# Kernel optimization log

Hardware: AMD Instinct MI355X
Metric: run time of the kernel (lower is better)

## Reference

```python
import jax, jax.numpy as jnp
import numpy as np

N, C, T, V = 16, 192, 120, 100
HEADS = 4
HEAD_CH = C // HEADS  # 48


def setup_inputs() -> dict:
    key = jax.random.key(0)
    ks = jax.random.split(key, 10)
    s = 0.05
    return {
        "x_q": jax.random.normal(ks[0], (N, C, T, V), jnp.float32),
        "x_kv": jax.random.normal(ks[1], (N, C, T, V), jnp.float32),
        "wq": jax.random.normal(ks[2], (C, C), jnp.float32) * s,
        "bq": jax.random.normal(ks[3], (C,), jnp.float32) * s,
        "wk": jax.random.normal(ks[4], (C, C), jnp.float32) * s,
        "bk": jax.random.normal(ks[5], (C,), jnp.float32) * s,
        "wp": jax.random.normal(ks[6], (C, C * HEADS), jnp.float32) * s,
        "bp": jax.random.normal(ks[7], (C,), jnp.float32) * s,
        "alphas": jnp.ones((1, HEADS, 1, 1), jnp.float32),
        "global_attn": jax.random.normal(ks[8], (1, 1, V, V), jnp.float32) * s,
    }


def reference(x_q, x_kv, wq, bq, wk, bk, wp, bp, alphas, global_attn):
    n, c, t, v = x_q.shape
    # 1x1 conv == pointwise linear over channel dim
    q = jnp.einsum('oc,nctv->notv', wq, x_q) + bq[None, :, None, None]
    k = jnp.einsum('oc,nctv->notv', wk, x_kv) + bk[None, :, None, None]
    q = q.reshape(n, HEADS, HEAD_CH, t, v)
    k = k.reshape(n, HEADS, HEAD_CH, t, v)
    # scores over (head_ch, T) contraction -> (N, heads, V, V)
    attn = jnp.tanh(jnp.einsum('nsctu,nsctv->nsuv', q, k) / (HEAD_CH * t))
    attn = attn * alphas + global_attn
    # aggregate full-channel x_kv per head: (N, heads, C, T, V)
    values = jnp.einsum('nctu,nsuv->nsctv', x_kv, attn)
    values = values.reshape(n, HEADS * c, t, v)
    out = jnp.einsum('oc,nctv->notv', wp, values) + bp[None, :, None, None]
    return out
```

## Files before the change

kernel.cpp:

```cpp
#include <hip/hip_runtime.h>

#define NN 16
#define CC 192
#define TT 120
#define VV 100
#define NH 4

typedef __attribute__((ext_vector_type(4))) float  float4v;
typedef __attribute__((ext_vector_type(8))) short  short8;
typedef __attribute__((ext_vector_type(2))) int    int2v;

#define MFMA16(A,B,Cacc) __builtin_amdgcn_mfma_f32_16x16x32_bf16(A,B,Cacc,0,0,0)

union S8U { unsigned u[4]; short8 s; };

__device__ __forceinline__ unsigned pk2(float a, float b) {
  union { float f; unsigned u; } x, y; x.f = a; y.f = b;
  return __builtin_amdgcn_perm(y.u, x.u, 0x07060302u);
}
__device__ __forceinline__ short b16t(float f) {
  union { float f; unsigned u; } x; x.f = f;
  return (short)(x.u >> 16);
}
__device__ __forceinline__ short f2b(float f) {
  union { float f; unsigned u; } x; x.f = f;
  unsigned r = x.u + 0x7fffu + ((x.u >> 16) & 1u);
  return (short)(r >> 16);
}

__global__ __launch_bounds__(256) void k_conv(const float* __restrict__ wq,
                                              const float* __restrict__ wk,
                                              const float* __restrict__ wp,
                                              short* __restrict__ wqF,
                                              short* __restrict__ wkF,
                                              short* __restrict__ wpF) {
  int i = blockIdx.x * 256 + threadIdx.x;
  if (i < CC*CC) {
    int o = i / CC, a = i % CC;
    int ct = o >> 4, l = o & 15, kc = a >> 5, q = (a & 31) >> 3, j = a & 7;
    int dst = ((ct*6 + kc)*64 + q*16 + l)*8 + j;
    wqF[dst] = f2b(wq[i]);
    wkF[dst] = f2b(wk[i]);
  }
  if (i < CC*CC*NH) {
    int o = i / (CC*NH), c2 = i % (CC*NH);
    int s = c2 / CC, cc = c2 % CC;
    int T = o >> 4, l = o & 15, kc = cc >> 5, q = (cc & 31) >> 3, j = cc & 7;
    int dst = (((s*12 + T)*6 + kc)*64 + q*16 + l)*8 + j;
    wpF[dst] = f2b(wp[i]);
  }
}

__global__ __launch_bounds__(448, 2) void k_qk(const float* __restrict__ xq,
                                               const float* __restrict__ xkv,
                                               const short* __restrict__ wqF,
                                               const short* __restrict__ wkF,
                                               const float* __restrict__ bq,
                                               const float* __restrict__ bk,
                                               short* __restrict__ Qf,
                                               short* __restrict__ Kf) {
  const int n = blockIdx.x / TT, t = blockIdx.x % TT;
  const int tid = threadIdx.x, w = tid >> 6, lane = tid & 63;
  const int q = lane >> 4, l15 = lane & 15;
  const int u = 16*w + l15, uc = (u < VV) ? u : (VV-1);
  const size_t ns0 = (size_t)n*NH;

  #pragma unroll 1
  for (int ph = 0; ph < 2; ++ph) {
    const float* xb   = (ph ? xkv : xq) + (size_t)n*CC*TT*VV + t*VV;
    const short* wF   = ph ? wkF : wqF;
    const float* bias = ph ? bk : bq;
    short*       Of   = ph ? Kf : Qf;

    short8 xf[6];
    #pragma unroll
    for (int kc = 0; kc < 6; ++kc) {
      float f[8];
      #pragma unroll
      for (int j = 0; j < 8; ++j)
        f[j] = xb[(size_t)(32*kc + 8*q + j)*(TT*VV) + uc];
      S8U sv; sv.u[0]=pk2(f[0],f[1]); sv.u[1]=pk2(f[2],f[3]); sv.u[2]=pk2(f[4],f[5]); sv.u[3]=pk2(f[6],f[7]);
      xf[kc] = sv.s;
    }
    #pragma unroll
    for (int ct = 0; ct < 12; ++ct) {
      float4v d = (float4v){0.f,0.f,0.f,0.f};
      #pragma unroll
      for (int kc = 0; kc < 6; ++kc) {
        short8 wf = *(const short8*)&wF[((ct*6 + kc)*64 + lane)*8];
        d = MFMA16(wf, xf[kc], d);
      }
      const float4v bv = *(const float4v*)&bias[16*ct + 4*q];
      const int sH = ct/3;
      const int kb = 48*t + 16*(ct - 3*sH);
      const int kq = kb + 4*q;
      const int kk = kq >> 5, q2 = (kq >> 3) & 3, j2 = kq & 7;
      size_t base = ((((ns0 + sH)*7 + w)*180 + kk)*64 + (q2*16 + l15))*8 + j2;
      #pragma unroll
      for (int r = 0; r < 4; ++r)
        Of[base + r] = b16t(d[r] + bv[r]);
    }
  }
}

__global__ __launch_bounds__(448, 2) void k_scores2(const short* __restrict__ Qf,
                                                    const short* __restrict__ Kf,
                                                    float* __restrict__ part2) {
  const int b = blockIdx.x;
  const int kc = b % 6, ns = b / 6;
  const int tid = threadIdx.x, w = tid >> 6, lane = tid & 63;
  const int q = lane >> 4, l15 = lane & 15;
  const short* Qb = Qf + (((size_t)ns*7 + w)*180 + kc*30)*512 + lane*8;
  const short* Kb = Kf + ((size_t)ns*7*180 + kc*30)*512 + lane*8;

  float4v acc[7];
  #pragma unroll
  for (int vt = 0; vt < 7; ++vt) acc[vt] = (float4v){0.f,0.f,0.f,0.f};

  #pragma unroll 2
  for (int kk = 0; kk < 30; ++kk) {
    short8 aQ = *(const short8*)&Qb[(size_t)kk*512];
    #pragma unroll
    for (int vt = 0; vt < 7; ++vt) {
      short8 bK = *(const short8*)&Kb[((size_t)vt*180 + kk)*512];
      acc[vt] = MFMA16(aQ, bK, acc[vt]);
    }
  }
  #pragma unroll
  for (int vt = 0; vt < 7; ++vt) {
    size_t p2 = (((size_t)ns*6 + kc)*112 + 16*vt + l15)*112 + 16*w + 4*q;
    __builtin_nontemporal_store(acc[vt], (float4v*)&part2[p2]);
  }
}

__global__ __launch_bounds__(256) void k_reduce2(const float* __restrict__ part2,
                                                 const float* __restrict__ alphas,
                                                 const float* __restrict__ ga,
                                                 short* __restrict__ attnT) {
  int bid = blockIdx.x;
  int ns = bid / 56, vc = bid % 56;
  int v = vc*2 + (threadIdx.x >> 7), u = threadIdx.x & 127;
  int s = ns & 3;
  float val = 0.f;
  if (v < VV && u < VV) {
    float sum = 0.f;
    #pragma unroll
    for (int kc = 0; kc < 6; ++kc)
      sum += __builtin_nontemporal_load(&part2[(((size_t)ns*6 + kc)*112 + v)*112 + u]);
    val = tanhf(sum * (1.f/5760.f)) * alphas[s] + ga[u*VV + v];
  }
  attnT[((size_t)ns*112 + v)*128 + u] = f2b(val);
}

__global__ __launch_bounds__(448, 2) void k_scoresB(const float* __restrict__ xq,
                                                    const float* __restrict__ xkv,
                                                    const short* __restrict__ wqF,
                                                    const short* __restrict__ wkF,
                                                    const float* __restrict__ bq,
                                                    const float* __restrict__ bk,
                                                    float* __restrict__ part) {
  __shared__ short QT[112*200];
  __shared__ short KT[112*56];
  const int n = blockIdx.x / 15, tc = blockIdx.x % 15;
  const int tid = threadIdx.x, w = tid >> 6, lane = tid & 63;
  const int q = lane >> 4, l15 = lane & 15;
  const int u = 16*w + l15, uc = (u < VV) ? u : (VV-1);
  float4v acc[NH][7];
  #pragma unroll
  for (int s = 0; s < NH; ++s)
    #pragma unroll
    for (int vt = 0; vt < 7; ++vt) acc[s][vt] = (float4v){0.f,0.f,0.f,0.f};
  const short8 z8 = {0,0,0,0,0,0,0,0};
  #pragma unroll 1
  for (int it = 0; it < 8; ++it) {
    const int t = tc*8 + it;
    short8 xf[6];
    #pragma unroll
    for (int kc = 0; kc < 6; ++kc) {
      float f[8];
      #pragma unroll
      for (int j = 0; j < 8; ++j)
        f[j] = xq[(n*CC + 32*kc + 8*q + j)*(TT*VV) + t*VV + uc];
      S8U sv; sv.u[0]=pk2(f[0],f[1]); sv.u[1]=pk2(f[2],f[3]); sv.u[2]=pk2(f[4],f[5]); sv.u[3]=pk2(f[6],f[7]);
      xf[kc] = sv.s;
    }
    #pragma unroll
    for (int ct = 0; ct < 12; ++ct) {
      float4v d = (float4v){0.f,0.f,0.f,0.f};
      #pragma unroll
      for (int kc = 0; kc < 6; ++kc) {
        short8 wf = *(const short8*)&wqF[((ct*6 + kc)*64 + q*16 + l15)*8];
        d = MFMA16(xf[kc], wf, d);
      }
      float bb = bq[16*ct + l15];
      #pragma unroll
      for (int r = 0; r < 4; ++r)
        QT[(16*w + 4*q + r)*200 + 16*ct + l15] = b16t(d[r] + bb);
    }
    short8 xg[6];
    #pragma unroll
    for (int kc = 0; kc < 6; ++kc) {
      float f[8];
      #pragma unroll
      for (int j = 0; j < 8; ++j)
        f[j] = xkv[(n*CC + 32*kc + 8*q + j)*(TT*VV) + t*VV + uc];
      S8U sv; sv.u[0]=pk2(f[0],f[1]); sv.u[1]=pk2(f[2],f[3]); sv.u[2]=pk2(f[4],f[5]); sv.u[3]=pk2(f[6],f[7]);
      xg[kc] = sv.s;
    }
    #pragma unroll 1
    for (int s = 0; s < NH; ++s) {
      #pragma unroll
      for (int ctk = 0; ctk < 3; ++ctk) {
        float4v d = (float4v){0.f,0.f,0.f,0.f};
        #pragma unroll
        for (int kc = 0; kc < 6; ++kc) {
          short8 wf = *(const short8*)&wkF[(((3*s + ctk)*6 + kc)*64 + q*16 + l15)*8];
          d = MFMA16(xg[kc], wf, d);
        }
        float bb = bk[48*s + 16*ctk + l15];
        #pragma unroll
        for (int r = 0; r < 4; ++r)
          KT[(16*w + 4*q + r)*56 + 16*ctk + l15] = b16t(d[r] + bb);
      }
      __syncthreads();
      #pragma unroll
      for (int kcp = 0; kcp < 2; ++kcp) {
        short8 aQ = z8;
        if (kcp == 0 || q < 2)
          aQ = *(const short8*)&QT[(16*w + l15)*200 + 48*s + 32*kcp + 8*q];
        #pragma unroll
        for (int vt = 0; vt < 7; ++vt) {
          short8 bK = z8;
          if (kcp == 0 || q < 2)
            bK = *(const short8*)&KT[(16*vt + l15)*56 + 32*kcp + 8*q];
          acc[s][vt] = MFMA16(aQ, bK, acc[s][vt]);
        }
      }
      __syncthreads();
    }
  }
  #pragma unroll
  for (int s = 0; s < NH; ++s)
    #pragma unroll
    for (int vt = 0; vt < 7; ++vt) {
      int v = 16*vt + l15;
      if (v < VV)
        __builtin_nontemporal_store(acc[s][vt],
          (float4v*)&part[(((n*15 + tc)*NH + s)*VV + v)*112 + 16*w + 4*q]);
    }
}

__global__ __launch_bounds__(256) void k_reduce(const float* __restrict__ part,
                                                const float* __restrict__ alphas,
                                                const float* __restrict__ ga,
                                                short* __restrict__ attnT) {
  int bid = blockIdx.x;
  int n = bid / 224, rem = bid % 224, s = rem / 56, vc = rem % 56;
  int v = vc*2 + (threadIdx.x >> 7), uu = threadIdx.x & 127;
  float val = 0.f;
  if (v < VV && uu < VV) {
    float sum = 0.f;
    for (int tcc = 0; tcc < 15; ++tcc)
      sum += __builtin_nontemporal_load(&part[(((n*15 + tcc)*NH + s)*VV + v)*112 + uu]);
    val = tanhf(sum * (1.f/5760.f)) * alphas[s] + ga[uu*VV + v];
  }
  attnT[((n*NH + s)*112 + v)*128 + uu] = f2b(val);
}

__global__ __launch_bounds__(256, 2) void k_outC(const float* __restrict__ xkv,
                                                 const short* __restrict__ wpF,
                                                 const short* __restrict__ attnT,
                                                 const float* __restrict__ bp,
                                                 float* __restrict__ out) {
  __shared__ short YT[112*200];
  const int n = blockIdx.x / TT, t = blockIdx.x % TT;
  const int tid = threadIdx.x, w = tid >> 6, lane = tid & 63;
  const int q = lane >> 4, l15 = lane & 15;

  float4v accO[3][7];
  #pragma unroll
  for (int i = 0; i < 3; ++i)
    #pragma unroll
    for (int vt = 0; vt < 7; ++vt) accO[i][vt] = (float4v){0.f,0.f,0.f,0.f};

  const float* xb[3];
  #pragma unroll
  for (int i = 0; i < 3; ++i) {
    int c = 16*(w + 4*i) + l15;
    xb[i] = xkv + ((size_t)(n*CC + c)*TT + t)*VV;
  }

  #pragma unroll 1
  for (int s = 0; s < NH; ++s) {
    float4v yacc[3][7];
    #pragma unroll
    for (int i = 0; i < 3; ++i)
      #pragma unroll
      for (int vt = 0; vt < 7; ++vt) yacc[i][vt] = (float4v){0.f,0.f,0.f,0.f};

    const short* aT = attnT + (size_t)((n*NH + s)*112)*128;

    #pragma unroll
    for (int ku = 0; ku < 4; ++ku) {
      short8 xa[3];
      #pragma unroll
      for (int i = 0; i < 3; ++i) {
        S8U sv;
        if (ku < 3) {
          const float4v A = *(const float4v*)(xb[i] + 32*ku + 8*q);
          const float4v B = *(const float4v*)(xb[i] + 32*ku + 8*q + 4);
          sv.u[0]=pk2(A[0],A[1]); sv.u[1]=pk2(A[2],A[3]);
          sv.u[2]=pk2(B[0],B[1]); sv.u[3]=pk2(B[2],B[3]);
        } else {
          if (q == 0) {
            const float4v A = *(const float4v*)(xb[i] + 96);
            sv.u[0]=pk2(A[0],A[1]); sv.u[1]=pk2(A[2],A[3]); sv.u[2]=0u; sv.u[3]=0u;
          } else {
            sv.u[0]=0u; sv.u[1]=0u; sv.u[2]=0u; sv.u[3]=0u;
          }
        }
        xa[i] = sv.s;
      }
      #pragma unroll
      for (int vt = 0; vt < 7; ++vt) {
        short8 bv = *(const short8*)&aT[(16*vt + l15)*128 + 32*ku + 8*q];
        #pragma unroll
        for (int i = 0; i < 3; ++i)
          yacc[i][vt] = MFMA16(xa[i], bv, yacc[i][vt]);
      }
    }

    __syncthreads();
    #pragma unroll
    for (int i = 0; i < 3; ++i)
      #pragma unroll
      for (int vt = 0; vt < 7; ++vt) {
        float4v d = yacc[i][vt];
        int2v pr; pr.x = (int)pk2(d[0], d[1]); pr.y = (int)pk2(d[2], d[3]);
        *(int2v*)&YT[(16*vt + l15)*200 + 16*(w + 4*i) + 4*q] = pr;
      }
    __syncthreads();

    #pragma unroll
    for (int kc2 = 0; kc2 < 6; ++kc2) {
      short8 ya[7];
      #pragma unroll
      for (int vt = 0; vt < 7; ++vt)
        ya[vt] = *(const short8*)&YT[(16*vt + l15)*200 + 32*kc2 + 8*q];
      #pragma unroll
      for (int i = 0; i < 3; ++i) {
        short8 wf = *(const short8*)&wpF[(((s*12 + (w + 4*i))*6 + kc2)*64 + q*16 + l15)*8];
        #pragma unroll
        for (int vt = 0; vt < 7; ++vt)
          accO[i][vt] = MFMA16(ya[vt], wf, accO[i][vt]);
      }
    }
  }

  #pragma unroll
  for (int i = 0; i < 3; ++i) {
    int o = 16*(w + 4*i) + l15;
    float b = bp[o];
    #pragma unroll
    for (int vt = 0; vt < 7; ++vt) {
      int v0 = 16*vt + 4*q;
      if (v0 < VV) {
        float4v r = accO[i][vt];
        r[0] += b; r[1] += b; r[2] += b; r[3] += b;
        __builtin_nontemporal_store(r, (float4v*)&out[((size_t)(n*CC + o)*TT + t)*VV + v0]);
      }
    }
  }
}

extern "C" void kernel_launch(void* const* d_in, const int* in_sizes, int n_in,
                              void* d_out, int out_size, void* d_ws, size_t ws_size,
                              hipStream_t stream) {
  const float* xq     = (const float*)d_in[0];
  const float* xkv    = (const float*)d_in[1];
  const float* wq     = (const float*)d_in[2];
  const float* bq     = (const float*)d_in[3];
  const float* wk     = (const float*)d_in[4];
  const float* bk     = (const float*)d_in[5];
  const float* wp     = (const float*)d_in[6];
  const float* bp     = (const float*)d_in[7];
  const float* alphas = (const float*)d_in[8];
  const float* ga     = (const float*)d_in[9];
  float* out = (float*)d_out;
  char*  ws  = (char*)d_ws;

  short* wqF   = (short*)(ws);
  short* wkF   = (short*)(ws + 73728);
  short* wpF   = (short*)(ws + 147456);
  short* attnT = (short*)(ws + 442368);

  hipLaunchKernelGGL(k_conv, dim3(576), dim3(256), 0, stream, wq, wk, wp, wqF, wkF, wpF);

  if (ws_size >= 186695680ULL) {
    short* Qf    = (short*)(ws + 2277376);
    short* Kf    = (short*)(ws + 84852736ULL);
    float* part2 = (float*)(ws + 167428096ULL);
    hipLaunchKernelGGL(k_qk,      dim3(1920), dim3(448), 0, stream, xq, xkv, wqF, wkF, bq, bk, Qf, Kf);
    hipLaunchKernelGGL(k_scores2, dim3(384),  dim3(448), 0, stream, Qf, Kf, part2);
    hipLaunchKernelGGL(k_reduce2, dim3(3584), dim3(256), 0, stream, part2, alphas, ga, attnT);
  } else {
    float* part = (float*)(ws + 2277376);
    hipLaunchKernelGGL(k_scoresB, dim3(240),  dim3(448), 0, stream, xq, xkv, wqF, wkF, bq, bk, part);
    hipLaunchKernelGGL(k_reduce,  dim3(3584), dim3(256), 0, stream, part, alphas, ga, attnT);
  }

  hipLaunchKernelGGL(k_outC, dim3(1920), dim3(256), 0, stream, xkv, wpF, attnT, bp, out);
}
```

Baseline: 899.0 us.

## Split scores over V halves, widen output kernel to 6 waves, vectorize Q/K stores

```diff
diff --git a/kernel.cpp b/kernel.cpp
--- a/kernel.cpp
+++ b/kernel.cpp
@@ -51,7 +51,7 @@
   }
 }
 
-__global__ __launch_bounds__(448, 2) void k_qk(const float* __restrict__ xq,
+__global__ __launch_bounds__(448, 3) void k_qk(const float* __restrict__ xq,
                                                const float* __restrict__ xkv,
                                                const short* __restrict__ wqF,
                                                const short* __restrict__ wkF,
@@ -96,40 +96,46 @@
       const int kq = kb + 4*q;
       const int kk = kq >> 5, q2 = (kq >> 3) & 3, j2 = kq & 7;
       size_t base = ((((ns0 + sH)*7 + w)*180 + kk)*64 + (q2*16 + l15))*8 + j2;
-      #pragma unroll
-      for (int r = 0; r < 4; ++r)
-        Of[base + r] = b16t(d[r] + bv[r]);
-    }
-  }
-}
-
-__global__ __launch_bounds__(448, 2) void k_scores2(const short* __restrict__ Qf,
+      int2v pr;
+      pr.x = (int)pk2(d[0] + bv[0], d[1] + bv[1]);
+      pr.y = (int)pk2(d[2] + bv[2], d[3] + bv[3]);
+      *(int2v*)&Of[base] = pr;
+    }
+  }
+}
+
+__global__ __launch_bounds__(448, 4) void k_scores3(const short* __restrict__ Qf,
                                                     const short* __restrict__ Kf,
                                                     float* __restrict__ part2) {
   const int b = blockIdx.x;
-  const int kc = b % 6, ns = b / 6;
+  const int vh = b & 1, kc = (b >> 1) % 6, ns = b / 12;
   const int tid = threadIdx.x, w = tid >> 6, lane = tid & 63;
   const int q = lane >> 4, l15 = lane & 15;
   const short* Qb = Qf + (((size_t)ns*7 + w)*180 + kc*30)*512 + lane*8;
   const short* Kb = Kf + ((size_t)ns*7*180 + kc*30)*512 + lane*8;
-
-  float4v acc[7];
-  #pragma unroll
-  for (int vt = 0; vt < 7; ++vt) acc[vt] = (float4v){0.f,0.f,0.f,0.f};
+  const int vt0 = vh ? 4 : 0, nvt = vh ? 3 : 4;
+
+  float4v acc[4];
+  #pragma unroll
+  for (int j = 0; j < 4; ++j) acc[j] = (float4v){0.f,0.f,0.f,0.f};
 
   #pragma unroll 2
   for (int kk = 0; kk < 30; ++kk) {
     short8 aQ = *(const short8*)&Qb[(size_t)kk*512];
     #pragma unroll
-    for (int vt = 0; vt < 7; ++vt) {
-      short8 bK = *(const short8*)&Kb[((size_t)vt*180 + kk)*512];
-      acc[vt] = MFMA16(aQ, bK, acc[vt]);
-    }
-  }
-  #pragma unroll
-  for (int vt = 0; vt < 7; ++vt) {
-    size_t p2 = (((size_t)ns*6 + kc)*112 + 16*vt + l15)*112 + 16*w + 4*q;
-    __builtin_nontemporal_store(acc[vt], (float4v*)&part2[p2]);
+    for (int j = 0; j < 4; ++j) {
+      if (j < nvt) {
+        short8 bK = *(const short8*)&Kb[((size_t)(vt0 + j)*180 + kk)*512];
+        acc[j] = MFMA16(aQ, bK, acc[j]);
+      }
+    }
+  }
+  #pragma unroll
+  for (int j = 0; j < 4; ++j) {
+    if (j < nvt) {
+      size_t p2 = (((size_t)ns*6 + kc)*112 + 16*(vt0 + j) + l15)*112 + 16*w + 4*q;
+      __builtin_nontemporal_store(acc[j], (float4v*)&part2[p2]);
+    }
   }
 }
 
@@ -267,7 +273,7 @@
   attnT[((n*NH + s)*112 + v)*128 + uu] = f2b(val);
 }
 
-__global__ __launch_bounds__(256, 2) void k_outC(const float* __restrict__ xkv,
+__global__ __launch_bounds__(384, 3) void k_outD(const float* __restrict__ xkv,
                                                  const short* __restrict__ wpF,
                                                  const short* __restrict__ attnT,
                                                  const float* __restrict__ bp,
@@ -277,68 +283,74 @@
   const int tid = threadIdx.x, w = tid >> 6, lane = tid & 63;
   const int q = lane >> 4, l15 = lane & 15;
 
-  float4v accO[3][7];
-  #pragma unroll
-  for (int i = 0; i < 3; ++i)
+  float4v accO[2][7];
+  #pragma unroll
+  for (int i = 0; i < 2; ++i)
     #pragma unroll
     for (int vt = 0; vt < 7; ++vt) accO[i][vt] = (float4v){0.f,0.f,0.f,0.f};
 
-  const float* xb[3];
-  #pragma unroll
-  for (int i = 0; i < 3; ++i) {
-    int c = 16*(w + 4*i) + l15;
-    xb[i] = xkv + ((size_t)(n*CC + c)*TT + t)*VV;
+  short8   xh[2][3];
+  unsigned xt[2][2];
+  #pragma unroll
+  for (int i = 0; i < 2; ++i) {
+    const float* xb = xkv + ((size_t)(n*CC + 16*(w + 6*i) + l15)*TT + t)*VV;
+    #pragma unroll
+    for (int ku = 0; ku < 3; ++ku) {
+      const float4v A = *(const float4v*)(xb + 32*ku + 8*q);
+      const float4v B = *(const float4v*)(xb + 32*ku + 8*q + 4);
+      S8U sv; sv.u[0]=pk2(A[0],A[1]); sv.u[1]=pk2(A[2],A[3]);
+      sv.u[2]=pk2(B[0],B[1]); sv.u[3]=pk2(B[2],B[3]);
+      xh[i][ku] = sv.s;
+    }
+    if (q == 0) {
+      const float4v A = *(const float4v*)(xb + 96);
+      xt[i][0] = pk2(A[0],A[1]); xt[i][1] = pk2(A[2],A[3]);
+    } else { xt[i][0] = 0u; xt[i][1] = 0u; }
   }
 
   #pragma unroll 1
   for (int s = 0; s < NH; ++s) {
-    float4v yacc[3][7];
-    #pragma unroll
-    for (int i = 0; i < 3; ++i)
-      #pragma unroll
-      for (int vt = 0; vt < 7; ++vt) yacc[i][vt] = (float4v){0.f,0.f,0.f,0.f};
-
     const short* aT = attnT + (size_t)((n*NH + s)*112)*128;
-
+    float4v y[7];
+
+    #pragma unroll
+    for (int vt = 0; vt < 7; ++vt) y[vt] = (float4v){0.f,0.f,0.f,0.f};
     #pragma unroll
     for (int ku = 0; ku < 4; ++ku) {
-      short8 xa[3];
-      #pragma unroll
-      for (int i = 0; i < 3; ++i) {
-        S8U sv;
-        if (ku < 3) {
-          const float4v A = *(const float4v*)(xb[i] + 32*ku + 8*q);
-          const float4v B = *(const float4v*)(xb[i] + 32*ku + 8*q + 4);
-          sv.u[0]=pk2(A[0],A[1]); sv.u[1]=pk2(A[2],A[3]);
-          sv.u[2]=pk2(B[0],B[1]); sv.u[3]=pk2(B[2],B[3]);
-        } else {
-          if (q == 0) {
-            const float4v A = *(const float4v*)(xb[i] + 96);
-            sv.u[0]=pk2(A[0],A[1]); sv.u[1]=pk2(A[2],A[3]); sv.u[2]=0u; sv.u[3]=0u;
-          } else {
-            sv.u[0]=0u; sv.u[1]=0u; sv.u[2]=0u; sv.u[3]=0u;
-          }
-        }
-        xa[i] = sv.s;
-      }
+      short8 xa;
+      if (ku < 3) xa = xh[0][ku];
+      else { S8U sv; sv.u[0]=xt[0][0]; sv.u[1]=xt[0][1]; sv.u[2]=0u; sv.u[3]=0u; xa = sv.s; }
       #pragma unroll
       for (int vt = 0; vt < 7; ++vt) {
         short8 bv = *(const short8*)&aT[(16*vt + l15)*128 + 32*ku + 8*q];
-        #pragma unroll
-        for (int i = 0; i < 3; ++i)
-          yacc[i][vt] = MFMA16(xa[i], bv, yacc[i][vt]);
-      }
-    }
-
+        y[vt] = MFMA16(xa, bv, y[vt]);
+      }
+    }
     __syncthreads();
     #pragma unroll
-    for (int i = 0; i < 3; ++i)
+    for (int vt = 0; vt < 7; ++vt) {
+      int2v pr; pr.x = (int)pk2(y[vt][0], y[vt][1]); pr.y = (int)pk2(y[vt][2], y[vt][3]);
+      *(int2v*)&YT[(16*vt + l15)*200 + 16*w + 4*q] = pr;
+    }
+
+    #pragma unroll
+    for (int vt = 0; vt < 7; ++vt) y[vt] = (float4v){0.f,0.f,0.f,0.f};
+    #pragma unroll
+    for (int ku = 0; ku < 4; ++ku) {
+      short8 xa;
+      if (ku < 3) xa = xh[1][ku];
+      else { S8U sv; sv.u[0]=xt[1][0]; sv.u[1]=xt[1][1]; sv.u[2]=0u; sv.u[3]=0u; xa = sv.s; }
       #pragma unroll
       for (int vt = 0; vt < 7; ++vt) {
-        float4v d = yacc[i][vt];
-        int2v pr; pr.x = (int)pk2(d[0], d[1]); pr.y = (int)pk2(d[2], d[3]);
-        *(int2v*)&YT[(16*vt + l15)*200 + 16*(w + 4*i) + 4*q] = pr;
-      }
+        short8 bv = *(const short8*)&aT[(16*vt + l15)*128 + 32*ku + 8*q];
+        y[vt] = MFMA16(xa, bv, y[vt]);
+      }
+    }
+    #pragma unroll
+    for (int vt = 0; vt < 7; ++vt) {
+      int2v pr; pr.x = (int)pk2(y[vt][0], y[vt][1]); pr.y = (int)pk2(y[vt][2], y[vt][3]);
+      *(int2v*)&YT[(16*vt + l15)*200 + 16*(w + 6) + 4*q] = pr;
+    }
     __syncthreads();
 
     #pragma unroll
@@ -348,8 +360,8 @@
       for (int vt = 0; vt < 7; ++vt)
         ya[vt] = *(const short8*)&YT[(16*vt + l15)*200 + 32*kc2 + 8*q];
       #pragma unroll
-      for (int i = 0; i < 3; ++i) {
-        short8 wf = *(const short8*)&wpF[(((s*12 + (w + 4*i))*6 + kc2)*64 + q*16 + l15)*8];
+      for (int i = 0; i < 2; ++i) {
+        short8 wf = *(const short8*)&wpF[(((s*12 + (w + 6*i))*6 + kc2)*64 + q*16 + l15)*8];
         #pragma unroll
         for (int vt = 0; vt < 7; ++vt)
           accO[i][vt] = MFMA16(ya[vt], wf, accO[i][vt]);
@@ -358,8 +370,8 @@
   }
 
   #pragma unroll
-  for (int i = 0; i < 3; ++i) {
-    int o = 16*(w + 4*i) + l15;
+  for (int i = 0; i < 2; ++i) {
+    int o = 16*(w + 6*i) + l15;
     float b = bp[o];
     #pragma unroll
     for (int vt = 0; vt < 7; ++vt) {
@@ -367,7 +379,7 @@
       if (v0 < VV) {
         float4v r = accO[i][vt];
         r[0] += b; r[1] += b; r[2] += b; r[3] += b;
-        __builtin_nontemporal_store(r, (float4v*)&out[((size_t)(n*CC + o)*TT + t)*VV + v0]);
+        *(float4v*)&out[((size_t)(n*CC + o)*TT + t)*VV + v0] = r;
       }
     }
   }
@@ -401,7 +413,7 @@
     short* Kf    = (short*)(ws + 84852736ULL);
     float* part2 = (float*)(ws + 167428096ULL);
     hipLaunchKernelGGL(k_qk,      dim3(1920), dim3(448), 0, stream, xq, xkv, wqF, wkF, bq, bk, Qf, Kf);
-    hipLaunchKernelGGL(k_scores2, dim3(384),  dim3(448), 0, stream, Qf, Kf, part2);
+    hipLaunchKernelGGL(k_scores3, dim3(768),  dim3(448), 0, stream, Qf, Kf, part2);
     hipLaunchKernelGGL(k_reduce2, dim3(3584), dim3(256), 0, stream, part2, alphas, ga, attnT);
   } else {
     float* part = (float*)(ws + 2277376);
@@ -409,5 +421,5 @@
     hipLaunchKernelGGL(k_reduce,  dim3(3584), dim3(256), 0, stream, part, alphas, ga, attnT);
   }
 
-  hipLaunchKernelGGL(k_outC, dim3(1920), dim3(256), 0, stream, xkv, wpF, attnT, bp, out);
-}
+  hipLaunchKernelGGL(k_outD, dim3(1920), dim3(384), 0, stream, xkv, wpF, attnT, bp, out);
+}
```

Measured after the change: 1.052 ms. +17.0%, slower.
